# Kernel optimization log

Hardware: AMD Instinct MI355X
Metric: run time of the kernel (lower is better)

The kernel has to match this reference:

```python
import jax, jax.numpy as jnp
import numpy as np

EMBED_DIM = 1024
BOTTLENECK = 48          # adapter_hidden_dim (adapter_rank=0)
ADAPTER_WIDTH = 1        # multivector channels
MV_DIM = 16              # Cl(1,3) multivector dimension
N_GRADES = 5             # grades of sizes 1,4,6,4,1
LN_EPS = 1e-5

# grade projection mask [5,16]: grade0=idx0, grade1=1:5, grade2=5:11, grade3=11:15, grade4=15
_gm = np.zeros((N_GRADES, MV_DIM), dtype=np.float32)
_gm[0, 0] = 1.0
_gm[1, 1:5] = 1.0
_gm[2, 5:11] = 1.0
_gm[3, 11:15] = 1.0
_gm[4, 15] = 1.0
GRADE_MASK = jnp.asarray(_gm)


def setup_inputs() -> dict:
    key = jax.random.key(0)
    ks = jax.random.split(key, 8)
    B, N, D, R, W = 128, 256, EMBED_DIM, BOTTLENECK, ADAPTER_WIDTH
    x = jax.random.normal(ks[0], (B, N, D), dtype=jnp.float32)
    gamma = jnp.ones((D,), dtype=jnp.float32)
    beta = jnp.zeros((D,), dtype=jnp.float32)
    w_down = jax.random.normal(ks[1], (R, D), dtype=jnp.float32) / np.sqrt(D)
    w_to_mv = jax.random.normal(ks[2], (W * MV_DIM, R), dtype=jnp.float32) / np.sqrt(R)
    w_equi = jax.random.normal(ks[3], (W, W, N_GRADES), dtype=jnp.float32)
    b_equi = jnp.zeros((W,), dtype=jnp.float32)
    w_from_mv = jax.random.normal(ks[4], (R, W * MV_DIM), dtype=jnp.float32) / np.sqrt(W * MV_DIM)
    w_up = jax.random.normal(ks[5], (D, R), dtype=jnp.float32) / np.sqrt(R)
    scale = jnp.float32(0.001)
    return {"x": x, "gamma": gamma, "beta": beta, "w_down": w_down,
            "w_to_mv": w_to_mv, "w_equi": w_equi, "b_equi": b_equi,
            "w_from_mv": w_from_mv, "w_up": w_up, "scale": scale}


def reference(x, gamma, beta, w_down, w_to_mv, w_equi, b_equi, w_from_mv, w_up, scale):
    B, N, D = x.shape
    # LayerNorm
    mu = jnp.mean(x, axis=-1, keepdims=True)
    var = jnp.mean(jnp.square(x - mu), axis=-1, keepdims=True)
    h = (x - mu) * jax.lax.rsqrt(var + LN_EPS) * gamma + beta
    # down + GELU (exact, matching torch F.gelu default)
    h = jax.nn.gelu(jnp.einsum('bnd,rd->bnr', h, w_down), approximate=False)
    # to multivectors [B,N,C,16]
    mv = jnp.einsum('bnr,mr->bnm', h, w_to_mv).reshape(B, N, -1, MV_DIM)
    # EquiLinear: per-grade channel mixing + scalar bias
    mv = jnp.einsum('oik,kj,bnij->bnoj', w_equi, GRADE_MASK, mv)
    mv = mv.at[..., 0].add(b_equi)
    # from multivectors + GELU
    h = jax.nn.gelu(jnp.einsum('bnm,rm->bnr', mv.reshape(B, N, -1), w_from_mv),
                    approximate=False)
    # up (dropout p=0 is identity) and scaled residual
    h = jnp.einsum('bnr,dr->bnd', h, w_up)
    return x + scale * h
```

## Files before the change

kernel.cpp:

```cpp
#include <hip/hip_runtime.h>
#include <hip/hip_bf16.h>


typedef __attribute__((ext_vector_type(8))) short short8;
typedef __attribute__((ext_vector_type(4))) short short4b;
typedef __attribute__((ext_vector_type(4))) float float4a;

#define TOKENS_PER_BLOCK 16
#define NTOK 32768
#define D 1024
#define R 48

__device__ __forceinline__ short f2bf(float x) {
    unsigned u = __float_as_uint(x);
    unsigned r = u + 0x7FFFu + ((u >> 16) & 1u);
    return (short)(r >> 16);
}
__device__ __forceinline__ float bf2f(short s) {
    return __uint_as_float(((unsigned)(unsigned short)s) << 16);
}
__device__ __forceinline__ float gelu_exact(float v) {
    return 0.5f * v * (1.0f + erff(v * 0.70710678118654752f));
}

__global__ void prep_weights(const float* __restrict__ wdn_f, const float* __restrict__ wup_f,
                             short* __restrict__ wdn_b, short* __restrict__ wup_b) {
    int o = blockIdx.x * 256 + threadIdx.x;
    if (o < 49152) {
        int j = o & 7, lane = (o >> 3) & 63, kt = (o >> 9) & 31, cb = o >> 14;
        int r = cb * 16 + (lane & 15);
        int d = kt * 32 + (lane >> 4) * 8 + j;
        wdn_b[o] = f2bf(wdn_f[r * 1024 + d]);
    } else {
        int o2 = o - 49152;
        if (o2 < 65536) {
            int j = o2 & 7, lane = (o2 >> 3) & 63, kt = (o2 >> 9) & 1, cb = o2 >> 10;
            int dcol = cb * 16 + (lane & 15);
            int r = kt * 32 + (lane >> 4) * 8 + j;
            wup_b[o2] = (r < 48) ? f2bf(wup_f[dcol * 48 + r]) : (short)0;
        }
    }
}

__launch_bounds__(256, 2)
__global__ void adapter_main(const float* __restrict__ x, const float* __restrict__ gamma,
                             const float* __restrict__ beta, const float* __restrict__ w_to_mv,
                             const float* __restrict__ w_equi, const float* __restrict__ b_equi,
                             const float* __restrict__ w_from_mv, const float* __restrict__ scale_p,
                             const short* __restrict__ wdn_b, const short* __restrict__ wup_b,
                             float* __restrict__ out) {
    __shared__ __align__(16) short hln[16][1032];
    __shared__ __align__(16) short xsh[16][1024];
    __shared__ __align__(16) float ypart[2][16][48];
    __shared__ __align__(16) float ybuf[16][48];
    __shared__ __align__(16) float mvbuf[16][16];
    __shared__ __align__(16) short zbuf[1024];

    const int tid  = threadIdx.x;
    const int lane = tid & 63;
    const int w    = tid >> 6;
    const int q    = lane >> 4;
    const int m    = lane & 15;
    const long token0 = (long)blockIdx.x * TOKENS_PER_BLOCK;

    zbuf[768 + tid] = 0;

    {
        const float4* g4 = (const float4*)gamma;
        const float4* b4 = (const float4*)beta;
        for (int t = 0; t < 4; ++t) {
            int tok = w * 4 + t;
            const float4* xr = (const float4*)(x + (token0 + tok) * D);
            float4 v[4];
            float s1 = 0.f, s2 = 0.f;
#pragma unroll
            for (int i = 0; i < 4; ++i) {
                v[i] = xr[lane + 64 * i];
                s1 += v[i].x + v[i].y + v[i].z + v[i].w;
                s2 += v[i].x * v[i].x + v[i].y * v[i].y + v[i].z * v[i].z + v[i].w * v[i].w;
            }
#pragma unroll
            for (int off = 32; off; off >>= 1) {
                s1 += __shfl_xor(s1, off);
                s2 += __shfl_xor(s2, off);
            }
            float mu = s1 * (1.0f / 1024.0f);
            float var = fmaf(-mu, mu, s2 * (1.0f / 1024.0f));
            float rs = rsqrtf(var + 1e-5f);
#pragma unroll
            for (int i = 0; i < 4; ++i) {
                int d0 = 4 * lane + 256 * i;
                float4 g = g4[lane + 64 * i];
                float4 b = b4[lane + 64 * i];
                float h0 = fmaf((v[i].x - mu) * rs, g.x, b.x);
                float h1 = fmaf((v[i].y - mu) * rs, g.y, b.y);
                float h2 = fmaf((v[i].z - mu) * rs, g.z, b.z);
                float h3 = fmaf((v[i].w - mu) * rs, g.w, b.w);
                short4b hs = {f2bf(h0), f2bf(h1), f2bf(h2), f2bf(h3)};
                *(short4b*)&hln[tok][d0] = hs;
                short4b xs = {f2bf(v[i].x), f2bf(v[i].y), f2bf(v[i].z), f2bf(v[i].w)};
                *(short4b*)&xsh[tok][d0] = xs;
            }
        }
    }
    __syncthreads();

#pragma unroll
    for (int rep = 0; rep < 2; ++rep) {
        int jid = w + rep * 4;
        if (jid < 6) {
            int cb = jid % 3, kh = jid / 3;
            float4a acc = {0.f, 0.f, 0.f, 0.f};
            const short* bptr = wdn_b + ((cb * 32 + kh * 16) * 64 + lane) * 8;
            const short* aptr = &hln[m][kh * 16 * 32 + q * 8];
#pragma unroll
            for (int kt = 0; kt < 16; ++kt) {
                short8 a = *(const short8*)(aptr + kt * 32);
                short8 b = *(const short8*)(bptr + kt * 512);
                acc = __builtin_amdgcn_mfma_f32_16x16x32_bf16(a, b, acc, 0, 0, 0);
            }
#pragma unroll
            for (int i = 0; i < 4; ++i) ypart[kh][q * 4 + i][cb * 16 + m] = acc[i];
        }
    }
    __syncthreads();

#pragma unroll
    for (int k = 0; k < 3; ++k) {
        int it = tid + k * 256;
        int tt = it / 48, r = it - tt * 48;
        float s = ypart[0][tt][r] + ypart[1][tt][r];
        ybuf[tt][r] = gelu_exact(s);
    }
    __syncthreads();
    {
        int tt = tid >> 4, j = tid & 15;
        float acc = 0.f;
#pragma unroll 8
        for (int r = 0; r < 48; ++r) acc = fmaf(w_to_mv[j * 48 + r], ybuf[tt][r], acc);
        int g = (j == 0) ? 0 : (j < 5) ? 1 : (j < 11) ? 2 : (j < 15) ? 3 : 4;
        acc *= w_equi[g];
        if (j == 0) acc += b_equi[0];
        mvbuf[tt][j] = acc;
    }
    __syncthreads();
#pragma unroll
    for (int k = 0; k < 3; ++k) {
        int it = tid + k * 256;
        int tt = it / 48, r = it - tt * 48;
        float acc = 0.f;
#pragma unroll
        for (int j = 0; j < 16; ++j) acc = fmaf(w_from_mv[r * 16 + j], mvbuf[tt][j], acc);
        float z = gelu_exact(acc);
        int kt = r >> 5, qq = (r >> 3) & 3, jj = r & 7;
        zbuf[kt * 512 + (qq * 16 + tt) * 8 + jj] = f2bf(z);
    }
    __syncthreads();

    const float scale = scale_p[0];
    short8 a0 = *(const short8*)&zbuf[lane * 8];
    short8 a1 = *(const short8*)&zbuf[512 + lane * 8];
    long rowbase = (token0 + q * 4) * D;
#pragma unroll 4
    for (int cc = 0; cc < 16; ++cc) {
        int cb = w * 16 + cc;
        short8 b0 = *(const short8*)(wup_b + (cb * 2 + 0) * 512 + lane * 8);
        short8 b1 = *(const short8*)(wup_b + (cb * 2 + 1) * 512 + lane * 8);
        float4a acc = {0.f, 0.f, 0.f, 0.f};
        acc = __builtin_amdgcn_mfma_f32_16x16x32_bf16(a0, b0, acc, 0, 0, 0);
        acc = __builtin_amdgcn_mfma_f32_16x16x32_bf16(a1, b1, acc, 0, 0, 0);
        int d = cb * 16 + m;
#pragma unroll
        for (int i = 0; i < 4; ++i) {
            int tok = q * 4 + i;
            float xv = bf2f(xsh[tok][d]);
            out[rowbase + (long)i * D + d] = fmaf(scale, acc[i], xv);
        }
    }
}

extern "C" void kernel_launch(void* const* d_in, const int* in_sizes, int n_in,
                              void* d_out, int out_size, void* d_ws, size_t ws_size,
                              hipStream_t stream) {
    const float* x         = (const float*)d_in[0];
    const float* gamma     = (const float*)d_in[1];
    const float* beta      = (const float*)d_in[2];
    const float* w_down    = (const float*)d_in[3];
    const float* w_to_mv   = (const float*)d_in[4];
    const float* w_equi    = (const float*)d_in[5];
    const float* b_equi    = (const float*)d_in[6];
    const float* w_from_mv = (const float*)d_in[7];
    const float* w_up      = (const float*)d_in[8];
    const float* scale_p   = (const float*)d_in[9];

    short* wdn_b = (short*)d_ws;
    short* wup_b = wdn_b + 49152;

    prep_weights<<<448, 256, 0, stream>>>(w_down, w_up, wdn_b, wup_b);
    adapter_main<<<NTOK / TOKENS_PER_BLOCK, 256, 0, stream>>>(
        x, gamma, beta, w_to_mv, w_equi, b_equi, w_from_mv, scale_p,
        wdn_b, wup_b, (float*)d_out);
}
```

Measured before the change: 269.7 us.

## Fold LayerNorm affine into down-projection and reuse raw x tile for MFMA

Gamma is folded into the bf16 down-projection weights, and the per-row sums W·gamma and W·beta are precomputed in the prep kernel. The main kernel now runs the down GEMM directly on the bf16 copy of raw x, then applies the per-token rs and -mu*rs corrections to the 48 outputs. This removes the separate normalized-activation LDS tile and shrinks shared memory so launch bounds can request 4 blocks per CU. All x loads for a wave are issued up front to raise memory-level parallelism. The trade-off is precision: the GEMM now sees un-centred bf16 x, so a large mean can cause cancellation error.

```diff
diff --git a/kernel.cpp b/kernel.cpp
--- a/kernel.cpp
+++ b/kernel.cpp
@@ -6,10 +6,8 @@
 typedef __attribute__((ext_vector_type(4))) short short4b;
 typedef __attribute__((ext_vector_type(4))) float float4a;
 
-#define TOKENS_PER_BLOCK 16
 #define NTOK 32768
 #define D 1024
-#define R 48
 
 __device__ __forceinline__ short f2bf(float x) {
     unsigned u = __float_as_uint(x);
@@ -24,82 +22,103 @@
 }
 
 __global__ void prep_weights(const float* __restrict__ wdn_f, const float* __restrict__ wup_f,
-                             short* __restrict__ wdn_b, short* __restrict__ wup_b) {
-    int o = blockIdx.x * 256 + threadIdx.x;
-    if (o < 49152) {
+                             const float* __restrict__ gamma, const float* __restrict__ beta,
+                             short* __restrict__ wdn_b, short* __restrict__ wup_b,
+                             float* __restrict__ c12) {
+    int blk = blockIdx.x;
+    int tid = threadIdx.x;
+    if (blk < 192) {
+        int o = blk * 256 + tid;
         int j = o & 7, lane = (o >> 3) & 63, kt = (o >> 9) & 31, cb = o >> 14;
         int r = cb * 16 + (lane & 15);
         int d = kt * 32 + (lane >> 4) * 8 + j;
-        wdn_b[o] = f2bf(wdn_f[r * 1024 + d]);
+        wdn_b[o] = f2bf(wdn_f[r * 1024 + d] * gamma[d]);
+    } else if (blk < 448) {
+        int o2 = (blk - 192) * 256 + tid;
+        int j = o2 & 7, lane = (o2 >> 3) & 63, kt = (o2 >> 9) & 1, cb = o2 >> 10;
+        int dcol = cb * 16 + (lane & 15);
+        int r = kt * 32 + (lane >> 4) * 8 + j;
+        wup_b[o2] = (r < 48) ? f2bf(wup_f[dcol * 48 + r]) : (short)0;
     } else {
-        int o2 = o - 49152;
-        if (o2 < 65536) {
-            int j = o2 & 7, lane = (o2 >> 3) & 63, kt = (o2 >> 9) & 1, cb = o2 >> 10;
-            int dcol = cb * 16 + (lane & 15);
-            int r = kt * 32 + (lane >> 4) * 8 + j;
-            wup_b[o2] = (r < 48) ? f2bf(wup_f[dcol * 48 + r]) : (short)0;
-        }
-    }
-}
-
-__launch_bounds__(256, 2)
-__global__ void adapter_main(const float* __restrict__ x, const float* __restrict__ gamma,
-                             const float* __restrict__ beta, const float* __restrict__ w_to_mv,
+        int r = blk - 448;
+        float a = 0.f, b = 0.f;
+#pragma unroll
+        for (int i = 0; i < 4; ++i) {
+            int d = tid + 256 * i;
+            float wv = wdn_f[r * 1024 + d];
+            a = fmaf(wv, gamma[d], a);
+            b = fmaf(wv, beta[d], b);
+        }
+#pragma unroll
+        for (int off = 32; off; off >>= 1) {
+            a += __shfl_xor(a, off);
+            b += __shfl_xor(b, off);
+        }
+        __shared__ float red[8];
+        int lane = tid & 63, w = tid >> 6;
+        if (lane == 0) { red[w] = a; red[4 + w] = b; }
+        __syncthreads();
+        if (tid == 0) {
+            c12[r]      = red[0] + red[1] + red[2] + red[3];
+            c12[48 + r] = red[4] + red[5] + red[6] + red[7];
+        }
+    }
+}
+
+__launch_bounds__(256, 4)
+__global__ void adapter_main(const float* __restrict__ x, const float* __restrict__ w_to_mv,
                              const float* __restrict__ w_equi, const float* __restrict__ b_equi,
                              const float* __restrict__ w_from_mv, const float* __restrict__ scale_p,
                              const short* __restrict__ wdn_b, const short* __restrict__ wup_b,
-                             float* __restrict__ out) {
-    __shared__ __align__(16) short hln[16][1032];
-    __shared__ __align__(16) short xsh[16][1024];
-    __shared__ __align__(16) float ypart[2][16][48];
-    __shared__ __align__(16) float ybuf[16][48];
-    __shared__ __align__(16) float mvbuf[16][16];
-    __shared__ __align__(16) short zbuf[1024];
+                             const float* __restrict__ c12, float* __restrict__ out) {
+    __shared__ __align__(16) short xsh[16][1032];
+    __shared__ __align__(16) float scratch[1568];
+    short* zbuf = (short*)scratch;
 
     const int tid  = threadIdx.x;
     const int lane = tid & 63;
     const int w    = tid >> 6;
     const int q    = lane >> 4;
     const int m    = lane & 15;
-    const long token0 = (long)blockIdx.x * TOKENS_PER_BLOCK;
-
-    zbuf[768 + tid] = 0;
+    const long token0 = (long)blockIdx.x * 16;
 
     {
-        const float4* g4 = (const float4*)gamma;
-        const float4* b4 = (const float4*)beta;
+        const float4* xr = (const float4*)(x + token0 * D);
+        float4 v[16];
+#pragma unroll
+        for (int t = 0; t < 4; ++t)
+#pragma unroll
+            for (int i = 0; i < 4; ++i)
+                v[t * 4 + i] = xr[(w * 4 + t) * 256 + lane + 64 * i];
+
+#pragma unroll
         for (int t = 0; t < 4; ++t) {
             int tok = w * 4 + t;
-            const float4* xr = (const float4*)(x + (token0 + tok) * D);
-            float4 v[4];
             float s1 = 0.f, s2 = 0.f;
 #pragma unroll
             for (int i = 0; i < 4; ++i) {
-                v[i] = xr[lane + 64 * i];
-                s1 += v[i].x + v[i].y + v[i].z + v[i].w;
-                s2 += v[i].x * v[i].x + v[i].y * v[i].y + v[i].z * v[i].z + v[i].w * v[i].w;
+                float4 vv = v[t * 4 + i];
+                s1 += vv.x + vv.y + vv.z + vv.w;
+                s2 += vv.x * vv.x + vv.y * vv.y + vv.z * vv.z + vv.w * vv.w;
             }
 #pragma unroll
             for (int off = 32; off; off >>= 1) {
                 s1 += __shfl_xor(s1, off);
                 s2 += __shfl_xor(s2, off);
             }
-            float mu = s1 * (1.0f / 1024.0f);
+            float mu  = s1 * (1.0f / 1024.0f);
             float var = fmaf(-mu, mu, s2 * (1.0f / 1024.0f));
-            float rs = rsqrtf(var + 1e-5f);
+            float rs  = rsqrtf(var + 1e-5f);
 #pragma unroll
             for (int i = 0; i < 4; ++i) {
                 int d0 = 4 * lane + 256 * i;
-                float4 g = g4[lane + 64 * i];
-                float4 b = b4[lane + 64 * i];
-                float h0 = fmaf((v[i].x - mu) * rs, g.x, b.x);
-                float h1 = fmaf((v[i].y - mu) * rs, g.y, b.y);
-                float h2 = fmaf((v[i].z - mu) * rs, g.z, b.z);
-                float h3 = fmaf((v[i].w - mu) * rs, g.w, b.w);
-                short4b hs = {f2bf(h0), f2bf(h1), f2bf(h2), f2bf(h3)};
-                *(short4b*)&hln[tok][d0] = hs;
-                short4b xs = {f2bf(v[i].x), f2bf(v[i].y), f2bf(v[i].z), f2bf(v[i].w)};
+                float4 vv = v[t * 4 + i];
+                short4b xs = {f2bf(vv.x), f2bf(vv.y), f2bf(vv.z), f2bf(vv.w)};
                 *(short4b*)&xsh[tok][d0] = xs;
+            }
+            if (lane == 0) {
+                scratch[1536 + tok] = rs;
+                scratch[1552 + tok] = -mu * rs;
             }
         }
     }
@@ -112,7 +131,7 @@
             int cb = jid % 3, kh = jid / 3;
             float4a acc = {0.f, 0.f, 0.f, 0.f};
             const short* bptr = wdn_b + ((cb * 32 + kh * 16) * 64 + lane) * 8;
-            const short* aptr = &hln[m][kh * 16 * 32 + q * 8];
+            const short* aptr = &xsh[m][kh * 512 + q * 8];
 #pragma unroll
             for (int kt = 0; kt < 16; ++kt) {
                 short8 a = *(const short8*)(aptr + kt * 32);
@@ -120,7 +139,8 @@
                 acc = __builtin_amdgcn_mfma_f32_16x16x32_bf16(a, b, acc, 0, 0, 0);
             }
 #pragma unroll
-            for (int i = 0; i < 4; ++i) ypart[kh][q * 4 + i][cb * 16 + m] = acc[i];
+            for (int i = 0; i < 4; ++i)
+                scratch[kh * 768 + (q * 4 + i) * 48 + cb * 16 + m] = acc[i];
         }
     }
     __syncthreads();
@@ -129,19 +149,20 @@
     for (int k = 0; k < 3; ++k) {
         int it = tid + k * 256;
         int tt = it / 48, r = it - tt * 48;
-        float s = ypart[0][tt][r] + ypart[1][tt][r];
-        ybuf[tt][r] = gelu_exact(s);
+        float s = scratch[tt * 48 + r] + scratch[768 + tt * 48 + r];
+        float y = fmaf(scratch[1536 + tt], s, fmaf(scratch[1552 + tt], c12[r], c12[48 + r]));
+        scratch[tt * 48 + r] = gelu_exact(y);
     }
     __syncthreads();
     {
         int tt = tid >> 4, j = tid & 15;
         float acc = 0.f;
 #pragma unroll 8
-        for (int r = 0; r < 48; ++r) acc = fmaf(w_to_mv[j * 48 + r], ybuf[tt][r], acc);
+        for (int r = 0; r < 48; ++r) acc = fmaf(w_to_mv[j * 48 + r], scratch[tt * 48 + r], acc);
         int g = (j == 0) ? 0 : (j < 5) ? 1 : (j < 11) ? 2 : (j < 15) ? 3 : 4;
         acc *= w_equi[g];
         if (j == 0) acc += b_equi[0];
-        mvbuf[tt][j] = acc;
+        scratch[768 + tt * 16 + j] = acc;
     }
     __syncthreads();
 #pragma unroll
@@ -150,11 +171,12 @@
         int tt = it / 48, r = it - tt * 48;
         float acc = 0.f;
 #pragma unroll
-        for (int j = 0; j < 16; ++j) acc = fmaf(w_from_mv[r * 16 + j], mvbuf[tt][j], acc);
+        for (int j = 0; j < 16; ++j) acc = fmaf(w_from_mv[r * 16 + j], scratch[768 + tt * 16 + j], acc);
         float z = gelu_exact(acc);
         int kt = r >> 5, qq = (r >> 3) & 3, jj = r & 7;
         zbuf[kt * 512 + (qq * 16 + tt) * 8 + jj] = f2bf(z);
     }
+    zbuf[768 + tid] = 0;
     __syncthreads();
 
     const float scale = scale_p[0];
@@ -195,9 +217,10 @@
 
     short* wdn_b = (short*)d_ws;
     short* wup_b = wdn_b + 49152;
-
-    prep_weights<<<448, 256, 0, stream>>>(w_down, w_up, wdn_b, wup_b);
-    adapter_main<<<NTOK / TOKENS_PER_BLOCK, 256, 0, stream>>>(
-        x, gamma, beta, w_to_mv, w_equi, b_equi, w_from_mv, scale_p,
-        wdn_b, wup_b, (float*)d_out);
-}
+    float* c12   = (float*)(wup_b + 65536);
+
+    prep_weights<<<496, 256, 0, stream>>>(w_down, w_up, gamma, beta, wdn_b, wup_b, c12);
+    adapter_main<<<NTOK / 16, 256, 0, stream>>>(
+        x, w_to_mv, w_equi, b_equi, w_from_mv, scale_p,
+        wdn_b, wup_b, c12, (float*)d_out);
+}
```

Result: faster. 262.8 us (-2.6%).
